# Kernel tuning notes

Hardware: AMD Instinct MI355X
Metric: run time of the kernel (lower is better)

The kernel has to match this reference:

```python
import jax, jax.numpy as jnp
import numpy as np

N_EMBD = 1024
N_HEAD = 16
HEAD_DIM = N_EMBD // N_HEAD
BLOCK_SIZE = 2048
ROPE_BASE = 10000.0


def _rope_tables(dim, max_len, base=ROPE_BASE):
    half = dim // 2
    freqs = 1.0 / base ** (jnp.arange(half, dtype=jnp.float32) / half)
    angles = jnp.arange(max_len, dtype=jnp.float32)[:, None] * freqs[None, :]  # (T, half)
    return jnp.cos(angles), jnp.sin(angles)


def _apply_rope(x, cos, sin):
    # x: (B, H, T, D); cos/sin: (T, D//2)
    T = x.shape[2]
    c = cos[:T][None, None]
    s = sin[:T][None, None]
    x1 = x[..., ::2]
    x2 = x[..., 1::2]
    out = jnp.stack([x1 * c - x2 * s, x1 * s + x2 * c], axis=-1)  # (B,H,T,D//2,2)
    return out.reshape(x.shape)


def setup_inputs() -> dict:
    key = jax.random.key(0)
    k1, k2, k3, k4, k5 = jax.random.split(key, 5)
    B, T, C = 2, 2048, N_EMBD
    x = jax.random.normal(k1, (B, T, C), dtype=jnp.float32)
    scale = 1.0 / np.sqrt(C)
    Wqkv = jax.random.normal(k2, (C, 3 * C), dtype=jnp.float32) * scale
    bqkv = jax.random.normal(k3, (3 * C,), dtype=jnp.float32) * 0.01
    Wproj = jax.random.normal(k4, (C, C), dtype=jnp.float32) * scale
    bproj = jax.random.normal(k5, (C,), dtype=jnp.float32) * 0.01
    cos, sin = _rope_tables(HEAD_DIM, BLOCK_SIZE)
    return {"x": x, "Wqkv": Wqkv, "bqkv": bqkv, "Wproj": Wproj, "bproj": bproj,
            "cos": cos, "sin": sin}


def reference(x, Wqkv, bqkv, Wproj, bproj, cos, sin):
    B, T, C = x.shape
    H, D = N_HEAD, HEAD_DIM
    qkv = x @ Wqkv + bqkv  # (B,T,3C)
    q, k, v = jnp.split(qkv, 3, axis=-1)
    # (B,T,C) -> (B,H,T,D)
    q = q.reshape(B, T, H, D).transpose(0, 2, 1, 3)
    k = k.reshape(B, T, H, D).transpose(0, 2, 1, 3)
    v = v.reshape(B, T, H, D).transpose(0, 2, 1, 3)
    q = _apply_rope(q, cos, sin)
    k = _apply_rope(k, cos, sin)
    att = jnp.einsum('bhtd,bhsd->bhts', q, k) * (D ** -0.5)
    causal = jnp.tril(jnp.ones((T, T), dtype=bool))
    att = jnp.where(causal[None, None], att, -jnp.inf)
    att = jax.nn.softmax(att, axis=-1)
    y = jnp.einsum('bhts,bhsd->bhtd', att, v)  # (B,H,T,D)
    y = y.transpose(0, 2, 1, 3).reshape(B, T, C)
    return y @ Wproj + bproj
```

## Files before the change

### kernel.cpp

```cpp
#include <hip/hip_runtime.h>
#include <stdint.h>

typedef short s16x8 __attribute__((ext_vector_type(8)));
typedef float f32x4 __attribute__((ext_vector_type(4)));
typedef unsigned short u16;
typedef unsigned int u32;

__device__ __forceinline__ float bf2f(u16 u) {
  union { u32 i; float f; } v; v.i = ((u32)u) << 16; return v.f;
}
__device__ __forceinline__ u16 f2bf(float f) {
  union { float f; u32 i; } v; v.f = f;
  u32 i = v.i;
  return (u16)((i + 0x7fffu + ((i >> 16) & 1u)) >> 16);
}
__device__ __forceinline__ u16 f2bf_fast(float f) {
  union { float f; u32 i; } v; v.f = f;
  return (u16)((v.i + 0x8000u) >> 16);
}

__device__ __forceinline__ s16x8 load8(const void* p, size_t idx, int isf32) {
  s16x8 r;
  if (isf32) {
    const float* f = (const float*)p + idx;
    f32x4 a = *(const f32x4*)f;
    f32x4 b = *(const f32x4*)(f + 4);
#pragma unroll
    for (int j = 0; j < 4; j++) {
      r[j] = (short)f2bf(a[j]);
      r[4 + j] = (short)f2bf(b[j]);
    }
  } else {
    r = *(const s16x8*)((const u16*)p + idx);
  }
  return r;
}
__device__ __forceinline__ float loadf(const void* p, size_t idx, int isf32) {
  return isf32 ? ((const float*)p)[idx] : bf2f(((const u16*)p)[idx]);
}

__device__ __forceinline__ void cp16(const u16* g, u16* l) {
  __builtin_amdgcn_global_load_lds(
      (const __attribute__((address_space(1))) u32*)g,
      (__attribute__((address_space(3))) u32*)l, 16, 0, 0);
}

__device__ __forceinline__ s16x8 rope8(s16x8 x, const float* c, const float* s) {
  s16x8 out;
#pragma unroll
  for (int j = 0; j < 4; j++) {
    float x1 = bf2f((u16)x[2 * j]);
    float x2 = bf2f((u16)x[2 * j + 1]);
    out[2 * j] = (short)f2bf(x1 * c[j] - x2 * s[j]);
    out[2 * j + 1] = (short)f2bf(x1 * s[j] + x2 * c[j]);
  }
  return out;
}

__global__ void detect_dtype(const u16* __restrict__ x, int* __restrict__ flags) {
  int cnt = 0;
  for (int i = threadIdx.x; i < 4096; i += 64) {
    int e = (x[i] >> 7) & 0xFF;
    if (e >= 0xF0) cnt++;
  }
  unsigned long long any = __ballot(cnt > 0);
  if (threadIdx.x == 0) {
    flags[0] = (any != 0ull) ? 1 : 0;
    flags[1] = 0;
  }
}

__global__ __launch_bounds__(256) void convert_x(const void* __restrict__ x,
                                                 const int* __restrict__ fp,
                                                 u16* __restrict__ xb) {
  size_t i = ((size_t)blockIdx.x * 256 + threadIdx.x) * 8;
  *(s16x8*)(xb + i) = load8(x, i, *fp);
}

__global__ __launch_bounds__(256) void transposeW2(
    const void* __restrict__ Wqkv, const void* __restrict__ Wproj,
    const int* __restrict__ fp, u16* __restrict__ WqkvT,
    u16* __restrict__ WprojT) {
  __shared__ u32 tile32[32 * 66];
  const int f = *fp;
  const int tid = threadIdx.x;
  const int bx = blockIdx.x;
  const void* W;
  u16* WT;
  int N, nb;
  if (bx < 48) { W = Wqkv; WT = WqkvT; N = 3072; nb = bx * 64; }
  else         { W = Wproj; WT = WprojT; N = 1024; nb = (bx - 48) * 64; }
  const int kb = blockIdx.y * 64;
  {
    int a = tid >> 3, c8 = tid & 7;
    s16x8 r0 = load8(W, (size_t)(kb + 2 * a) * N + nb + c8 * 8, f);
    s16x8 r1 = load8(W, (size_t)(kb + 2 * a + 1) * N + nb + c8 * 8, f);
#pragma unroll
    for (int j = 0; j < 8; j++)
      tile32[a * 66 + c8 * 8 + j] = (u32)(u16)r0[j] | ((u32)(u16)r1[j] << 16);
  }
  __syncthreads();
#pragma unroll
  for (int i = 0; i < 2; i++) {
    int idx = tid + i * 256;
    int n = idx >> 3, c8 = idx & 7;
    s16x8 v;
#pragma unroll
    for (int w = 0; w < 4; w++) {
      u32 pk = tile32[(c8 * 4 + w) * 66 + n];
      v[2 * w] = (short)(u16)(pk & 0xFFFF);
      v[2 * w + 1] = (short)(u16)(pk >> 16);
    }
    *(s16x8*)(WT + (size_t)(nb + n) * 1024 + kb + c8 * 8) = v;
  }
}

__global__ __launch_bounds__(256) void postproc(u16* __restrict__ qkv,
                                                u16* __restrict__ vT,
                                                const void* __restrict__ cost,
                                                const void* __restrict__ sint,
                                                const int* __restrict__ fp) {
  __shared__ u32 tile32[64 * 33];
  const int f = *fp;
  const int tid = threadIdx.x;
  const int tb = blockIdx.x * 64, bh = blockIdx.y;
  const int b = bh >> 4, h = bh & 15;

  {
    int a = tid >> 3, c8 = tid & 7;
    const u16* base = qkv + (size_t)(b * 2048 + tb + 2 * a) * 3072 + 2048 + h * 64;
    s16x8 r0 = *(const s16x8*)(base + c8 * 8);
    s16x8 r1 = *(const s16x8*)(base + 3072 + c8 * 8);
#pragma unroll
    for (int j = 0; j < 8; j++)
      tile32[(c8 * 8 + j) * 33 + a] = (u32)(u16)r0[j] | ((u32)(u16)r1[j] << 16);
  }

#pragma unroll
  for (int g = 0; g < 2; g++) {
    int gi = tid + g * 256;
    int row = gi >> 3, c8 = gi & 7;
    int t = tb + row;
    size_t base = (size_t)(b * 2048 + t) * 3072 + h * 64 + c8 * 8;
    float cc[4], ss[4];
    if (f) {
      f32x4 cv = *(const f32x4*)((const float*)cost + (size_t)t * 32 + c8 * 4);
      f32x4 sv = *(const f32x4*)((const float*)sint + (size_t)t * 32 + c8 * 4);
#pragma unroll
      for (int k = 0; k < 4; k++) { cc[k] = cv[k]; ss[k] = sv[k]; }
    } else {
#pragma unroll
      for (int k = 0; k < 4; k++) {
        cc[k] = bf2f(((const u16*)cost)[(size_t)t * 32 + c8 * 4 + k]);
        ss[k] = bf2f(((const u16*)sint)[(size_t)t * 32 + c8 * 4 + k]);
      }
    }
    s16x8 q = *(const s16x8*)(qkv + base);
    *(s16x8*)(qkv + base) = rope8(q, cc, ss);
    s16x8 kk = *(const s16x8*)(qkv + base + 1024);
    *(s16x8*)(qkv + base + 1024) = rope8(kk, cc, ss);
  }

  __syncthreads();
#pragma unroll
  for (int i = 0; i < 2; i++) {
    int idx = tid + i * 256;
    int d = idx >> 3, c8 = idx & 7;
    s16x8 v;
#pragma unroll
    for (int w = 0; w < 4; w++) {
      u32 pk = tile32[d * 33 + c8 * 4 + w];
      v[2 * w] = (short)(u16)(pk & 0xFFFF);
      v[2 * w + 1] = (short)(u16)(pk >> 16);
    }
    *(s16x8*)(vT + ((size_t)bh * 64 + d) * 2048 + tb + c8 * 8) = v;
  }
}

template <int NT>
__global__ __launch_bounds__(256) void gemm_bt(
    const u16* __restrict__ A, int lda, const u16* __restrict__ Bt,
    const void* __restrict__ bias, const int* __restrict__ fI32,
    void* __restrict__ C, int outF, int N, int K) {
  constexpr int NTW = NT / 32;
  constexpr int CS = NT + 4;
  constexpr int STAGE = 128 * 32 + NT * 32;
  constexpr int SMSZ = (STAGE > 64 * CS) ? STAGE : 64 * CS;
  __shared__ __attribute__((aligned(16))) u16 SMEM[SMSZ];
  u16* As = SMEM;
  u16* Bs = SMEM + 128 * 32;
  const int inf32 = *fI32;
  const int tid = threadIdx.x;
  const int wave = tid >> 6, lane = tid & 63, quad = lane >> 4, l16 = lane & 15;
  const int m0 = blockIdx.y * 128, n0 = blockIdx.x * NT;
  const int wm = (wave & 1) * 64, wn = (wave >> 1) * (NT / 2);
  const int lr = lane >> 2, lk = (lane & 3) * 8;
  f32x4 acc[4][NTW];
#pragma unroll
  for (int i = 0; i < 4; i++)
#pragma unroll
    for (int j = 0; j < NTW; j++) acc[i][j] = (f32x4){0.f, 0.f, 0.f, 0.f};

  const u16* aP = A + (size_t)(m0 + wave * 32 + lr) * lda + lk;
  const u16* bP = Bt + (size_t)(n0 + wave * (NT / 4) + lr) * K + lk;
  u16* asl = As + wave * 32 * 32;
  u16* bsl = Bs + wave * (NT / 4) * 32;

  for (int kb = 0; kb < K; kb += 32) {
    __syncthreads();
    cp16(aP + kb, asl);
    cp16(aP + kb + (size_t)16 * lda, asl + 16 * 32);
#pragma unroll
    for (int i = 0; i < NT / 64; i++)
      cp16(bP + kb + (size_t)(16 * i) * K, bsl + i * 16 * 32);
    __syncthreads();
    s16x8 af[4], bfr[NTW];
#pragma unroll
    for (int t = 0; t < 4; t++)
      af[t] = *(const s16x8*)(As + (wm + t * 16 + l16) * 32 + quad * 8);
#pragma unroll
    for (int t = 0; t < NTW; t++)
      bfr[t] = *(const s16x8*)(Bs + (wn + t * 16 + l16) * 32 + quad * 8);
#pragma unroll
    for (int mt = 0; mt < 4; mt++)
#pragma unroll
      for (int nt = 0; nt < NTW; nt++)
        acc[mt][nt] = __builtin_amdgcn_mfma_f32_16x16x32_bf16(
            af[mt], bfr[nt], acc[mt][nt], 0, 0, 0);
  }

  float bv[NTW];
#pragma unroll
  for (int nt = 0; nt < NTW; nt++)
    bv[nt] = loadf(bias, n0 + wn + nt * 16 + l16, inf32);

  if (outF && inf32) {
#pragma unroll
    for (int nt = 0; nt < NTW; nt++) {
      int col = n0 + wn + nt * 16 + l16;
#pragma unroll
      for (int mt = 0; mt < 4; mt++)
#pragma unroll
        for (int r = 0; r < 4; r++) {
          int row = m0 + wm + mt * 16 + quad * 4 + r;
          ((float*)C)[(size_t)row * N + col] = acc[mt][nt][r] + bv[nt];
        }
    }
    return;
  }

  u16* Cs = SMEM;
#pragma unroll
  for (int half = 0; half < 2; half++) {
    __syncthreads();
    if ((wave & 1) == half) {
#pragma unroll
      for (int mt = 0; mt < 4; mt++)
#pragma unroll
        for (int nt = 0; nt < NTW; nt++)
#pragma unroll
          for (int r = 0; r < 4; r++)
            Cs[(mt * 16 + quad * 4 + r) * CS + wn + nt * 16 + l16] =
                f2bf(acc[mt][nt][r] + bv[nt]);
    }
    __syncthreads();
    int row = tid >> 2, cg = tid & 3;
    int colbase = cg * (NT / 4);
    u16* gout = (u16*)C + (size_t)(m0 + half * 64 + row) * N + n0 + colbase;
    const u16* lsrc = Cs + row * CS + colbase;
#pragma unroll
    for (int k2 = 0; k2 < NT / 32; k2++)
      *(s16x8*)(gout + k2 * 8) = *(const s16x8*)(lsrc + k2 * 8);
  }
}

__global__ __launch_bounds__(512) void attn_kernel(u16* qkv,
                                                   const u16* __restrict__ vT) {
  __shared__ __attribute__((aligned(16))) u16 Ks[64 * 72];
  __shared__ __attribute__((aligned(16))) u16 Vt[64 * 72];
  __shared__ __attribute__((aligned(16))) u16 Pl[8][16 * 72];
  const int tid = threadIdx.x;
  const int wave = tid >> 6, lane = tid & 63, quad = lane >> 4, l16 = lane & 15;
  const int cu = blockIdx.x & 255, round = blockIdx.x >> 8;
  const int p = cu >> 5, bh = cu & 31;
  const int qt = round ? p : 15 - p;
  const int h = bh & 15;
  const size_t rb = (size_t)(bh >> 4) * 2048;
  const int qb = qt * 128;
  const float SCALE = 0.18033688011112042f;

  s16x8 qa0, qa1;
  {
    const u16* qp = qkv + (rb + qb + wave * 16 + l16) * 3072 + h * 64;
    qa0 = *(const s16x8*)(qp + quad * 8);
    qa1 = *(const s16x8*)(qp + 32 + quad * 8);
  }

  f32x4 o[4];
  float l_r[4] = {0.f, 0.f, 0.f, 0.f};
#pragma unroll
  for (int i = 0; i < 4; i++) o[i] = (f32x4){0.f, 0.f, 0.f, 0.f};

  const int nchunks = 2 * qt + 2;
  const int srow = tid >> 3, sc8 = tid & 7;
  s16x8 kr, vr;
  {
    kr = *(const s16x8*)(qkv + (rb + srow) * 3072 + 1024 + h * 64 + sc8 * 8);
    vr = *(const s16x8*)(vT + ((size_t)bh * 64 + srow) * 2048 + sc8 * 8);
  }

  for (int c = 0; c < nchunks; c++) {
    const int sb = c * 64;
    __syncthreads();
    *(s16x8*)(Ks + srow * 72 + sc8 * 8) = kr;
    *(s16x8*)(Vt + srow * 72 + sc8 * 8) = vr;
    __syncthreads();
    if (c + 1 < nchunks) {
      const int nb = sb + 64;
      kr = *(const s16x8*)(qkv + (rb + nb + srow) * 3072 + 1024 + h * 64 +
                           sc8 * 8);
      vr = *(const s16x8*)(vT + ((size_t)bh * 64 + srow) * 2048 + nb + sc8 * 8);
    }

    if (sb > qb + wave * 16 + 15) continue;

    f32x4 S[4];
#pragma unroll
    for (int kf = 0; kf < 4; kf++) {
      s16x8 k0 = *(const s16x8*)(Ks + (kf * 16 + l16) * 72 + quad * 8);
      s16x8 k1 = *(const s16x8*)(Ks + (kf * 16 + l16) * 72 + 32 + quad * 8);
      f32x4 a = (f32x4){0.f, 0.f, 0.f, 0.f};
      a = __builtin_amdgcn_mfma_f32_16x16x32_bf16(qa0, k0, a, 0, 0, 0);
      a = __builtin_amdgcn_mfma_f32_16x16x32_bf16(qa1, k1, a, 0, 0, 0);
      S[kf] = a;
    }

    u16* P = Pl[wave];
    const int mq = qb + wave * 16;
    const bool needMask = (sb + 63) > mq;
#pragma unroll
    for (int r = 0; r < 4; r++) {
      const int qi = mq + quad * 4 + r;
#pragma unroll
      for (int kf = 0; kf < 4; kf++) {
        float pv = __builtin_amdgcn_exp2f(S[kf][r] * SCALE);
        if (needMask) pv = ((sb + kf * 16 + l16) <= qi) ? pv : 0.f;
        l_r[r] += pv;
        P[(quad * 4 + r) * 72 + kf * 16 + l16] = f2bf_fast(pv);
      }
    }
    asm volatile("s_waitcnt lgkmcnt(0)" ::: "memory");
    s16x8 pa0 = *(const s16x8*)(P + l16 * 72 + quad * 8);
    s16x8 pa1 = *(const s16x8*)(P + l16 * 72 + 32 + quad * 8);

#pragma unroll
    for (int dt = 0; dt < 4; dt++) {
      s16x8 vb0 = *(const s16x8*)(Vt + (dt * 16 + l16) * 72 + quad * 8);
      s16x8 vb1 = *(const s16x8*)(Vt + (dt * 16 + l16) * 72 + 32 + quad * 8);
      o[dt] = __builtin_amdgcn_mfma_f32_16x16x32_bf16(pa0, vb0, o[dt], 0, 0, 0);
      o[dt] = __builtin_amdgcn_mfma_f32_16x16x32_bf16(pa1, vb1, o[dt], 0, 0, 0);
    }
  }

  float inv[4];
#pragma unroll
  for (int r = 0; r < 4; r++) {
    float rs = l_r[r];
#pragma unroll
    for (int off = 8; off; off >>= 1) rs += __shfl_xor(rs, off);
    inv[r] = 1.0f / fmaxf(rs, 1e-30f);
  }
#pragma unroll
  for (int dt = 0; dt < 4; dt++)
#pragma unroll
    for (int r = 0; r < 4; r++)
      qkv[(rb + qb + wave * 16 + quad * 4 + r) * 3072 + 2048 + h * 64 +
          dt * 16 + l16] = f2bf(o[dt][r] * inv[r]);
}

extern "C" void kernel_launch(void* const* d_in, const int* in_sizes, int n_in,
                              void* d_out, int out_size, void* d_ws,
                              size_t ws_size, hipStream_t stream) {
  const void* x = d_in[0];
  const void* Wqkv = d_in[1];
  const void* bqkv = d_in[2];
  const void* Wproj = d_in[3];
  const void* bproj = d_in[4];
  const void* cost = d_in[5];
  const void* sint = d_in[6];

  int* flags = (int*)d_ws;
  u16* WqkvT = (u16*)d_ws + 128;
  u16* WprojT = WqkvT + (size_t)3072 * 1024;
  u16* qkv = WprojT + (size_t)1024 * 1024;
  u16* yb = qkv + 2048;
  u16* xb = (u16*)d_out;
  u16* vT = (u16*)d_out + (size_t)4096 * 1024;

  detect_dtype<<<1, 64, 0, stream>>>((const u16*)x, flags);
  convert_x<<<2048, 256, 0, stream>>>(x, flags, xb);
  transposeW2<<<dim3(64, 16), 256, 0, stream>>>(Wqkv, Wproj, flags, WqkvT,
                                                WprojT);
  gemm_bt<128><<<dim3(24, 32), 256, 0, stream>>>(xb, 1024, WqkvT, bqkv, flags,
                                                 qkv, 0, 3072, 1024);
  postproc<<<dim3(32, 32), 256, 0, stream>>>(qkv, vT, cost, sint, flags);
  attn_kernel<<<512, 512, 0, stream>>>(qkv, vT);
  gemm_bt<64><<<dim3(16, 32), 256, 0, stream>>>(yb, 3072, WprojT, bproj, flags,
                                                d_out, 1, 1024, 1024);
}
```

Before: 212.3 us.

## Drop dtype detection, fuse prep kernels, RoPE in GEMM epilogue, double-buffer attention K/V

Removes the runtime dtype detection and assumes fp32 inputs. Merges the x conversion and weight transposes into one prep launch. Applies RoPE inside the QKV GEMM epilogue, so postproc now only transposes V. Double-buffers K/V tiles in shared memory in the attention kernel, which removes one barrier per chunk and overlaps the LDS stores with compute. Together this cuts two kernel launches and one read-modify-write pass over q/k, at the cost of more LDS in attention and losing support for bf16 inputs.

```diff
diff --git a/kernel.cpp b/kernel.cpp
--- a/kernel.cpp
+++ b/kernel.cpp
@@ -6,6 +6,7 @@
 typedef unsigned short u16;
 typedef unsigned int u32;
 
+
 __device__ __forceinline__ float bf2f(u16 u) {
   union { u32 i; float f; } v; v.i = ((u32)u) << 16; return v.f;
 }
@@ -19,24 +20,16 @@
   return (u16)((v.i + 0x8000u) >> 16);
 }
 
-__device__ __forceinline__ s16x8 load8(const void* p, size_t idx, int isf32) {
+__device__ __forceinline__ s16x8 load8f(const float* f) {
+  f32x4 a = *(const f32x4*)f;
+  f32x4 b = *(const f32x4*)(f + 4);
   s16x8 r;
-  if (isf32) {
-    const float* f = (const float*)p + idx;
-    f32x4 a = *(const f32x4*)f;
-    f32x4 b = *(const f32x4*)(f + 4);
-#pragma unroll
-    for (int j = 0; j < 4; j++) {
-      r[j] = (short)f2bf(a[j]);
-      r[4 + j] = (short)f2bf(b[j]);
-    }
-  } else {
-    r = *(const s16x8*)((const u16*)p + idx);
+#pragma unroll
+  for (int j = 0; j < 4; j++) {
+    r[j] = (short)f2bf(a[j]);
+    r[4 + j] = (short)f2bf(b[j]);
   }
   return r;
-}
-__device__ __forceinline__ float loadf(const void* p, size_t idx, int isf32) {
-  return isf32 ? ((const float*)p)[idx] : bf2f(((const u16*)p)[idx]);
 }
 
 __device__ __forceinline__ void cp16(const u16* g, u16* l) {
@@ -45,56 +38,31 @@
       (__attribute__((address_space(3))) u32*)l, 16, 0, 0);
 }
 
-__device__ __forceinline__ s16x8 rope8(s16x8 x, const float* c, const float* s) {
-  s16x8 out;
-#pragma unroll
-  for (int j = 0; j < 4; j++) {
-    float x1 = bf2f((u16)x[2 * j]);
-    float x2 = bf2f((u16)x[2 * j + 1]);
-    out[2 * j] = (short)f2bf(x1 * c[j] - x2 * s[j]);
-    out[2 * j + 1] = (short)f2bf(x1 * s[j] + x2 * c[j]);
-  }
-  return out;
-}
-
-__global__ void detect_dtype(const u16* __restrict__ x, int* __restrict__ flags) {
-  int cnt = 0;
-  for (int i = threadIdx.x; i < 4096; i += 64) {
-    int e = (x[i] >> 7) & 0xFF;
-    if (e >= 0xF0) cnt++;
-  }
-  unsigned long long any = __ballot(cnt > 0);
-  if (threadIdx.x == 0) {
-    flags[0] = (any != 0ull) ? 1 : 0;
-    flags[1] = 0;
-  }
-}
-
-__global__ __launch_bounds__(256) void convert_x(const void* __restrict__ x,
-                                                 const int* __restrict__ fp,
-                                                 u16* __restrict__ xb) {
-  size_t i = ((size_t)blockIdx.x * 256 + threadIdx.x) * 8;
-  *(s16x8*)(xb + i) = load8(x, i, *fp);
-}
-
-__global__ __launch_bounds__(256) void transposeW2(
-    const void* __restrict__ Wqkv, const void* __restrict__ Wproj,
-    const int* __restrict__ fp, u16* __restrict__ WqkvT,
-    u16* __restrict__ WprojT) {
+__global__ __launch_bounds__(256) void prep(const float* __restrict__ x,
+                                            const float* __restrict__ Wqkv,
+                                            const float* __restrict__ Wproj,
+                                            u16* __restrict__ xb,
+                                            u16* __restrict__ WqkvT,
+                                            u16* __restrict__ WprojT) {
   __shared__ u32 tile32[32 * 66];
-  const int f = *fp;
   const int tid = threadIdx.x;
-  const int bx = blockIdx.x;
-  const void* W;
+  int bx = blockIdx.x;
+  if (bx < 2048) {
+    size_t i = ((size_t)bx * 256 + tid) * 8;
+    *(s16x8*)(xb + i) = load8f(x + i);
+    return;
+  }
+  bx -= 2048;
+  const int bn = bx & 63, kb = (bx >> 6) * 64;
+  const float* W;
   u16* WT;
   int N, nb;
-  if (bx < 48) { W = Wqkv; WT = WqkvT; N = 3072; nb = bx * 64; }
-  else         { W = Wproj; WT = WprojT; N = 1024; nb = (bx - 48) * 64; }
-  const int kb = blockIdx.y * 64;
+  if (bn < 48) { W = Wqkv; WT = WqkvT; N = 3072; nb = bn * 64; }
+  else         { W = Wproj; WT = WprojT; N = 1024; nb = (bn - 48) * 64; }
   {
     int a = tid >> 3, c8 = tid & 7;
-    s16x8 r0 = load8(W, (size_t)(kb + 2 * a) * N + nb + c8 * 8, f);
-    s16x8 r1 = load8(W, (size_t)(kb + 2 * a + 1) * N + nb + c8 * 8, f);
+    s16x8 r0 = load8f(W + (size_t)(kb + 2 * a) * N + nb + c8 * 8);
+    s16x8 r1 = load8f(W + (size_t)(kb + 2 * a + 1) * N + nb + c8 * 8);
 #pragma unroll
     for (int j = 0; j < 8; j++)
       tile32[a * 66 + c8 * 8 + j] = (u32)(u16)r0[j] | ((u32)(u16)r1[j] << 16);
@@ -115,17 +83,12 @@
   }
 }
 
-__global__ __launch_bounds__(256) void postproc(u16* __restrict__ qkv,
-                                                u16* __restrict__ vT,
-                                                const void* __restrict__ cost,
-                                                const void* __restrict__ sint,
-                                                const int* __restrict__ fp) {
+__global__ __launch_bounds__(256) void transposeV(const u16* __restrict__ qkv,
+                                                  u16* __restrict__ vT) {
   __shared__ u32 tile32[64 * 33];
-  const int f = *fp;
   const int tid = threadIdx.x;
   const int tb = blockIdx.x * 64, bh = blockIdx.y;
   const int b = bh >> 4, h = bh & 15;
-
   {
     int a = tid >> 3, c8 = tid & 7;
     const u16* base = qkv + (size_t)(b * 2048 + tb + 2 * a) * 3072 + 2048 + h * 64;
@@ -135,32 +98,6 @@
     for (int j = 0; j < 8; j++)
       tile32[(c8 * 8 + j) * 33 + a] = (u32)(u16)r0[j] | ((u32)(u16)r1[j] << 16);
   }
-
-#pragma unroll
-  for (int g = 0; g < 2; g++) {
-    int gi = tid + g * 256;
-    int row = gi >> 3, c8 = gi & 7;
-    int t = tb + row;
-    size_t base = (size_t)(b * 2048 + t) * 3072 + h * 64 + c8 * 8;
-    float cc[4], ss[4];
-    if (f) {
-      f32x4 cv = *(const f32x4*)((const float*)cost + (size_t)t * 32 + c8 * 4);
-      f32x4 sv = *(const f32x4*)((const float*)sint + (size_t)t * 32 + c8 * 4);
-#pragma unroll
-      for (int k = 0; k < 4; k++) { cc[k] = cv[k]; ss[k] = sv[k]; }
-    } else {
-#pragma unroll
-      for (int k = 0; k < 4; k++) {
-        cc[k] = bf2f(((const u16*)cost)[(size_t)t * 32 + c8 * 4 + k]);
-        ss[k] = bf2f(((const u16*)sint)[(size_t)t * 32 + c8 * 4 + k]);
-      }
-    }
-    s16x8 q = *(const s16x8*)(qkv + base);
-    *(s16x8*)(qkv + base) = rope8(q, cc, ss);
-    s16x8 kk = *(const s16x8*)(qkv + base + 1024);
-    *(s16x8*)(qkv + base + 1024) = rope8(kk, cc, ss);
-  }
-
   __syncthreads();
 #pragma unroll
   for (int i = 0; i < 2; i++) {
@@ -180,8 +117,9 @@
 template <int NT>
 __global__ __launch_bounds__(256) void gemm_bt(
     const u16* __restrict__ A, int lda, const u16* __restrict__ Bt,
-    const void* __restrict__ bias, const int* __restrict__ fI32,
-    void* __restrict__ C, int outF, int N, int K) {
+    const float* __restrict__ bias, void* __restrict__ C, int outF,
+    int ropeMode, const float* __restrict__ cost,
+    const float* __restrict__ sint, int N, int K) {
   constexpr int NTW = NT / 32;
   constexpr int CS = NT + 4;
   constexpr int STAGE = 128 * 32 + NT * 32;
@@ -189,7 +127,6 @@
   __shared__ __attribute__((aligned(16))) u16 SMEM[SMSZ];
   u16* As = SMEM;
   u16* Bs = SMEM + 128 * 32;
-  const int inf32 = *fI32;
   const int tid = threadIdx.x;
   const int wave = tid >> 6, lane = tid & 63, quad = lane >> 4, l16 = lane & 15;
   const int m0 = blockIdx.y * 128, n0 = blockIdx.x * NT;
@@ -231,10 +168,9 @@
 
   float bv[NTW];
 #pragma unroll
-  for (int nt = 0; nt < NTW; nt++)
-    bv[nt] = loadf(bias, n0 + wn + nt * 16 + l16, inf32);
-
-  if (outF && inf32) {
+  for (int nt = 0; nt < NTW; nt++) bv[nt] = bias[n0 + wn + nt * 16 + l16];
+
+  if (outF) {
 #pragma unroll
     for (int nt = 0; nt < NTW; nt++) {
       int col = n0 + wn + nt * 16 + l16;
@@ -249,6 +185,7 @@
     return;
   }
 
+  const bool doRope = ropeMode && (n0 < 2048);
   u16* Cs = SMEM;
 #pragma unroll
   for (int half = 0; half < 2; half++) {
@@ -268,16 +205,38 @@
     int colbase = cg * (NT / 4);
     u16* gout = (u16*)C + (size_t)(m0 + half * 64 + row) * N + n0 + colbase;
     const u16* lsrc = Cs + row * CS + colbase;
-#pragma unroll
-    for (int k2 = 0; k2 < NT / 32; k2++)
-      *(s16x8*)(gout + k2 * 8) = *(const s16x8*)(lsrc + k2 * 8);
+    if (doRope) {
+      int t = (m0 + half * 64 + row) & 2047;
+      int j0 = (colbase & 63) >> 1;
+      const float* cp = cost + (size_t)t * 32 + j0;
+      const float* sp = sint + (size_t)t * 32 + j0;
+#pragma unroll
+      for (int k2 = 0; k2 < NT / 32; k2++) {
+        s16x8 v = *(const s16x8*)(lsrc + k2 * 8);
+        f32x4 cv = *(const f32x4*)(cp + k2 * 4);
+        f32x4 sv = *(const f32x4*)(sp + k2 * 4);
+        s16x8 o;
+#pragma unroll
+        for (int j = 0; j < 4; j++) {
+          float x1 = bf2f((u16)v[2 * j]);
+          float x2 = bf2f((u16)v[2 * j + 1]);
+          o[2 * j] = (short)f2bf(x1 * cv[j] - x2 * sv[j]);
+          o[2 * j + 1] = (short)f2bf(x1 * sv[j] + x2 * cv[j]);
+        }
+        *(s16x8*)(gout + k2 * 8) = o;
+      }
+    } else {
+#pragma unroll
+      for (int k2 = 0; k2 < NT / 32; k2++)
+        *(s16x8*)(gout + k2 * 8) = *(const s16x8*)(lsrc + k2 * 8);
+    }
   }
 }
 
 __global__ __launch_bounds__(512) void attn_kernel(u16* qkv,
                                                    const u16* __restrict__ vT) {
-  __shared__ __attribute__((aligned(16))) u16 Ks[64 * 72];
-  __shared__ __attribute__((aligned(16))) u16 Vt[64 * 72];
+  __shared__ __attribute__((aligned(16))) u16 Ks[2][64 * 72];
+  __shared__ __attribute__((aligned(16))) u16 Vt[2][64 * 72];
   __shared__ __attribute__((aligned(16))) u16 Pl[8][16 * 72];
   const int tid = threadIdx.x;
   const int wave = tid >> 6, lane = tid & 63, quad = lane >> 4, l16 = lane & 15;
@@ -303,18 +262,17 @@
 
   const int nchunks = 2 * qt + 2;
   const int srow = tid >> 3, sc8 = tid & 7;
+  const int myqhi = qb + wave * 16 + 15;
   s16x8 kr, vr;
-  {
-    kr = *(const s16x8*)(qkv + (rb + srow) * 3072 + 1024 + h * 64 + sc8 * 8);
-    vr = *(const s16x8*)(vT + ((size_t)bh * 64 + srow) * 2048 + sc8 * 8);
-  }
+  kr = *(const s16x8*)(qkv + (rb + srow) * 3072 + 1024 + h * 64 + sc8 * 8);
+  vr = *(const s16x8*)(vT + ((size_t)bh * 64 + srow) * 2048 + sc8 * 8);
+  *(s16x8*)(Ks[0] + srow * 72 + sc8 * 8) = kr;
+  *(s16x8*)(Vt[0] + srow * 72 + sc8 * 8) = vr;
+  __syncthreads();
 
   for (int c = 0; c < nchunks; c++) {
     const int sb = c * 64;
-    __syncthreads();
-    *(s16x8*)(Ks + srow * 72 + sc8 * 8) = kr;
-    *(s16x8*)(Vt + srow * 72 + sc8 * 8) = vr;
-    __syncthreads();
+    const int cur = c & 1;
     if (c + 1 < nchunks) {
       const int nb = sb + 64;
       kr = *(const s16x8*)(qkv + (rb + nb + srow) * 3072 + 1024 + h * 64 +
@@ -322,44 +280,54 @@
       vr = *(const s16x8*)(vT + ((size_t)bh * 64 + srow) * 2048 + nb + sc8 * 8);
     }
 
-    if (sb > qb + wave * 16 + 15) continue;
-
-    f32x4 S[4];
-#pragma unroll
-    for (int kf = 0; kf < 4; kf++) {
-      s16x8 k0 = *(const s16x8*)(Ks + (kf * 16 + l16) * 72 + quad * 8);
-      s16x8 k1 = *(const s16x8*)(Ks + (kf * 16 + l16) * 72 + 32 + quad * 8);
-      f32x4 a = (f32x4){0.f, 0.f, 0.f, 0.f};
-      a = __builtin_amdgcn_mfma_f32_16x16x32_bf16(qa0, k0, a, 0, 0, 0);
-      a = __builtin_amdgcn_mfma_f32_16x16x32_bf16(qa1, k1, a, 0, 0, 0);
-      S[kf] = a;
-    }
-
-    u16* P = Pl[wave];
-    const int mq = qb + wave * 16;
-    const bool needMask = (sb + 63) > mq;
-#pragma unroll
-    for (int r = 0; r < 4; r++) {
-      const int qi = mq + quad * 4 + r;
+    if (sb <= myqhi) {
+      f32x4 S[4];
 #pragma unroll
       for (int kf = 0; kf < 4; kf++) {
-        float pv = __builtin_amdgcn_exp2f(S[kf][r] * SCALE);
-        if (needMask) pv = ((sb + kf * 16 + l16) <= qi) ? pv : 0.f;
-        l_r[r] += pv;
-        P[(quad * 4 + r) * 72 + kf * 16 + l16] = f2bf_fast(pv);
+        s16x8 k0 = *(const s16x8*)(Ks[cur] + (kf * 16 + l16) * 72 + quad * 8);
+        s16x8 k1 =
+            *(const s16x8*)(Ks[cur] + (kf * 16 + l16) * 72 + 32 + quad * 8);
+        f32x4 a = (f32x4){0.f, 0.f, 0.f, 0.f};
+        a = __builtin_amdgcn_mfma_f32_16x16x32_bf16(qa0, k0, a, 0, 0, 0);
+        a = __builtin_amdgcn_mfma_f32_16x16x32_bf16(qa1, k1, a, 0, 0, 0);
+        S[kf] = a;
       }
-    }
-    asm volatile("s_waitcnt lgkmcnt(0)" ::: "memory");
-    s16x8 pa0 = *(const s16x8*)(P + l16 * 72 + quad * 8);
-    s16x8 pa1 = *(const s16x8*)(P + l16 * 72 + 32 + quad * 8);
-
-#pragma unroll
-    for (int dt = 0; dt < 4; dt++) {
-      s16x8 vb0 = *(const s16x8*)(Vt + (dt * 16 + l16) * 72 + quad * 8);
-      s16x8 vb1 = *(const s16x8*)(Vt + (dt * 16 + l16) * 72 + 32 + quad * 8);
-      o[dt] = __builtin_amdgcn_mfma_f32_16x16x32_bf16(pa0, vb0, o[dt], 0, 0, 0);
-      o[dt] = __builtin_amdgcn_mfma_f32_16x16x32_bf16(pa1, vb1, o[dt], 0, 0, 0);
-    }
+
+      u16* P = Pl[wave];
+      const int mq = qb + wave * 16;
+      const bool needMask = (sb + 63) > mq;
+#pragma unroll
+      for (int r = 0; r < 4; r++) {
+        const int qi = mq + quad * 4 + r;
+#pragma unroll
+        for (int kf = 0; kf < 4; kf++) {
+          float pv = __builtin_amdgcn_exp2f(S[kf][r] * SCALE);
+          if (needMask) pv = ((sb + kf * 16 + l16) <= qi) ? pv : 0.f;
+          l_r[r] += pv;
+          P[(quad * 4 + r) * 72 + kf * 16 + l16] = f2bf_fast(pv);
+        }
+      }
+      asm volatile("s_waitcnt lgkmcnt(0)" ::: "memory");
+      s16x8 pa0 = *(const s16x8*)(P + l16 * 72 + quad * 8);
+      s16x8 pa1 = *(const s16x8*)(P + l16 * 72 + 32 + quad * 8);
+
+#pragma unroll
+      for (int dt = 0; dt < 4; dt++) {
+        s16x8 vb0 = *(const s16x8*)(Vt[cur] + (dt * 16 + l16) * 72 + quad * 8);
+        s16x8 vb1 =
+            *(const s16x8*)(Vt[cur] + (dt * 16 + l16) * 72 + 32 + quad * 8);
+        o[dt] =
+            __builtin_amdgcn_mfma_f32_16x16x32_bf16(pa0, vb0, o[dt], 0, 0, 0);
+        o[dt] =
+            __builtin_amdgcn_mfma_f32_16x16x32_bf16(pa1, vb1, o[dt], 0, 0, 0);
+      }
+    }
+
+    if (c + 1 < nchunks) {
+      *(s16x8*)(Ks[cur ^ 1] + srow * 72 + sc8 * 8) = kr;
+      *(s16x8*)(Vt[cur ^ 1] + srow * 72 + sc8 * 8) = vr;
+    }
+    __syncthreads();
   }
 
   float inv[4];
@@ -381,30 +349,26 @@
 extern "C" void kernel_launch(void* const* d_in, const int* in_sizes, int n_in,
                               void* d_out, int out_size, void* d_ws,
                               size_t ws_size, hipStream_t stream) {
-  const void* x = d_in[0];
-  const void* Wqkv = d_in[1];
-  const void* bqkv = d_in[2];
-  const void* Wproj = d_in[3];
-  const void* bproj = d_in[4];
-  const void* cost = d_in[5];
-  const void* sint = d_in[6];
-
-  int* flags = (int*)d_ws;
-  u16* WqkvT = (u16*)d_ws + 128;
+  const float* x = (const float*)d_in[0];
+  const float* Wqkv = (const float*)d_in[1];
+  const float* bqkv = (const float*)d_in[2];
+  const float* Wproj = (const float*)d_in[3];
+  const float* bproj = (const float*)d_in[4];
+  const float* cost = (const float*)d_in[5];
+  const float* sint = (const float*)d_in[6];
+
+  u16* WqkvT = (u16*)d_ws;
   u16* WprojT = WqkvT + (size_t)3072 * 1024;
   u16* qkv = WprojT + (size_t)1024 * 1024;
   u16* yb = qkv + 2048;
   u16* xb = (u16*)d_out;
   u16* vT = (u16*)d_out + (size_t)4096 * 1024;
 
-  detect_dtype<<<1, 64, 0, stream>>>((const u16*)x, flags);
-  convert_x<<<2048, 256, 0, stream>>>(x, flags, xb);
-  transposeW2<<<dim3(64, 16), 256, 0, stream>>>(Wqkv, Wproj, flags, WqkvT,
-                                                WprojT);
-  gemm_bt<128><<<dim3(24, 32), 256, 0, stream>>>(xb, 1024, WqkvT, bqkv, flags,
-                                                 qkv, 0, 3072, 1024);
-  postproc<<<dim3(32, 32), 256, 0, stream>>>(qkv, vT, cost, sint, flags);
+  prep<<<3072, 256, 0, stream>>>(x, Wqkv, Wproj, xb, WqkvT, WprojT);
+  gemm_bt<128><<<dim3(24, 32), 256, 0, stream>>>(
+      xb, 1024, WqkvT, bqkv, qkv, 0, 1, cost, sint, 3072, 1024);
+  transposeV<<<dim3(32, 32), 256, 0, stream>>>(qkv, vT);
   attn_kernel<<<512, 512, 0, stream>>>(qkv, vT);
-  gemm_bt<64><<<dim3(16, 32), 256, 0, stream>>>(yb, 3072, WprojT, bproj, flags,
-                                                d_out, 1, 1024, 1024);
-}
+  gemm_bt<64><<<dim3(16, 32), 256, 0, stream>>>(
+      yb, 3072, WprojT, bproj, d_out, 1, 0, nullptr, nullptr, 1024, 1024);
+}
```

Measured after the change: 214.8 us. Within noise of the previous version (+1.2%).
